# Kernel tuning notes

Hardware: AMD Instinct MI355X
Metric: run time of the kernel (lower is better)

Reference implementation:

```python
import jax, jax.numpy as jnp
import numpy as np

IN_F = 1024
OUT_F = 4096
SEARCH_SPACE = [1, 2, 4, 8, 16]  # block sizes; powers of 2 dividing both dims, capped at 16


def circ_avg(W, bs):
    """Project W [out,in] onto block-circulant structure with block size bs.

    Equivalent to trans_to_cir_meng: within each (bs x bs) block, average each
    wrap-around diagonal and rebuild a circulant block C[k, j] = c[(k - j) % bs].
    """
    q, p = W.shape[0] // bs, W.shape[1] // bs
    t = W.reshape(q, bs, p, bs).transpose(0, 2, 1, 3)  # [q, p, bs, bs]
    i = jnp.arange(bs)
    # rot[..., i, j] = t[..., i, (i + j) % bs]  (rotate rows so diagonals align in columns)
    rot = t[:, :, i[:, None], (i[:, None] + i[None, :]) % bs]  # [q, p, bs, bs]
    c = rot.mean(axis=2)  # [q, p, bs]  mean over each diagonal
    # circulant block: w[..., k, j] = c[..., (k - j) % bs]
    w = c[:, :, (i[:, None] - i[None, :]) % bs]  # [q, p, bs, bs]
    return w.transpose(0, 2, 1, 3).reshape(W.shape)


def setup_inputs() -> dict:
    key = jax.random.key(0)
    k1, k2, k3, k4 = jax.random.split(key, 4)
    x = jax.random.normal(k1, (16, 512, IN_F), dtype=jnp.float32)
    weight = jax.random.normal(k2, (OUT_F, IN_F), dtype=jnp.float32) * 0.02
    alphas = jax.random.normal(k3, (len(SEARCH_SPACE),), dtype=jnp.float32)
    bias = jax.random.normal(k4, (OUT_F,), dtype=jnp.float32) * 0.02
    return {"x": x, "weight": weight, "alphas": alphas, "bias": bias}


def reference(x, weight, alphas, bias):
    # soft NAS mixture over block sizes (tau=1, soft mode)
    a = jax.nn.softmax(alphas)
    W = a[0] * weight  # block_size 1 == original weight
    for idx, bs in enumerate(SEARCH_SPACE[1:], start=1):
        W = W + a[idx] * circ_avg(weight, bs)
    # F.linear: y = x @ W^T + b
    return jnp.einsum("bsi,oi->bso", x, W) + bias
```

## Files before the change

### kernel.cpp

```cpp
#include <hip/hip_runtime.h>

typedef __bf16 bf16;
typedef __bf16 bf16x8 __attribute__((ext_vector_type(8)));
typedef float floatx4 __attribute__((ext_vector_type(4)));

#define IN_F  1024
#define OUT_F 4096
#define M_DIM 8192
#define K_DIM 1024
#define N_DIM 4096

__device__ __forceinline__ unsigned short f2bf(float f) {
    unsigned int u = __float_as_uint(f);
    u += 0x7FFFu + ((u >> 16) & 1u);
    return (unsigned short)(u >> 16);
}

__global__ __launch_bounds__(256) void build_w_kernel(
    const float* __restrict__ W, const float* __restrict__ alphas,
    unsigned short* __restrict__ Wb)
{
    __shared__ __align__(16) float Wl[16 * 256];
    __shared__ __align__(16) float D2[2048];
    __shared__ float D4[1024];
    __shared__ float D8[512];
    __shared__ float D16[256];

    const int t = threadIdx.x;
    const int rb = blockIdx.x >> 2;
    const int cb = blockIdx.x & 3;
    const int row0 = rb * 16, col0 = cb * 256;

    const float4* src = (const float4*)(W + (size_t)row0 * IN_F + col0);
    #pragma unroll
    for (int j = 0; j < 4; ++j) {
        const int idx = j * 256 + t;
        const int r = idx >> 6, c4 = idx & 63;
        ((float4*)Wl)[r * 64 + c4] = src[(size_t)r * 256 + c4];
    }

    float av[5];
    float mx = -1e30f;
    #pragma unroll
    for (int j = 0; j < 5; ++j) { av[j] = alphas[j]; mx = fmaxf(mx, av[j]); }
    float s = 0.f;
    #pragma unroll
    for (int j = 0; j < 5; ++j) { av[j] = __expf(av[j] - mx); s += av[j]; }
    const float inv = 1.f / s;
    #pragma unroll
    for (int j = 0; j < 5; ++j) av[j] *= inv;
    #pragma unroll
    for (int e = 1; e <= 4; ++e) av[e] *= 1.0f / (float)(1 << e);

    __syncthreads();

    {
        const int c16 = t >> 4, d = t & 15;
        float acc = 0.f;
        #pragma unroll
        for (int r = 0; r < 16; ++r)
            acc += Wl[r * 256 + c16 * 16 + ((r + d) & 15)];
        D16[t] = acc;
    }
    #pragma unroll
    for (int it = 0; it < 2; ++it) {
        const int s8 = t + it * 256;
        const int d = s8 & 7, c8 = (s8 >> 3) & 31, r8 = s8 >> 8;
        float acc = 0.f;
        #pragma unroll
        for (int r = 0; r < 8; ++r)
            acc += Wl[(r8 * 8 + r) * 256 + c8 * 8 + ((r + d) & 7)];
        D8[s8] = acc;
    }
    #pragma unroll
    for (int it = 0; it < 4; ++it) {
        const int s4 = t + it * 256;
        const int d = s4 & 3, c4 = (s4 >> 2) & 63, r4 = s4 >> 8;
        float acc = 0.f;
        #pragma unroll
        for (int r = 0; r < 4; ++r)
            acc += Wl[(r4 * 4 + r) * 256 + c4 * 4 + ((r + d) & 3)];
        D4[s4] = acc;
    }
    #pragma unroll
    for (int it = 0; it < 8; ++it) {
        const int s2 = t + it * 256;
        const int d = s2 & 1, c2 = (s2 >> 1) & 127, r2 = s2 >> 8;
        D2[s2] = Wl[(r2 * 2) * 256 + c2 * 2 + d]
               + Wl[(r2 * 2 + 1) * 256 + c2 * 2 + ((1 + d) & 1)];
    }

    __syncthreads();

    const int k = t >> 4, jj = t & 15;
    float res[16];
    #pragma unroll
    for (int jb = 0; jb < 16; ++jb) {
        const int col = jb * 16 + jj;
        const int dd = k - col;
        res[jb] = av[0] * Wl[k * 256 + col]
                + av[1] * D2[((k >> 1) * 128 + (col >> 1)) * 2 + (dd & 1)]
                + av[2] * D4[((k >> 2) * 64  + (col >> 2)) * 4 + (dd & 3)]
                + av[3] * D8[((k >> 3) * 32  + (col >> 3)) * 8 + (dd & 7)]
                + av[4] * D16[(col >> 4) * 16 + (dd & 15)];
    }

    __syncthreads();
    unsigned short* st = (unsigned short*)D2;
    #pragma unroll
    for (int jb = 0; jb < 16; ++jb)
        st[k * 256 + jb * 16 + jj] = f2bf(res[jb]);
    __syncthreads();

    const uint4* p = (const uint4*)(st + k * 256 + jj * 16);
    uint4* dst = (uint4*)(Wb + (size_t)(row0 + k) * IN_F + col0 + jj * 16);
    dst[0] = p[0];
    dst[1] = p[1];
}

__global__ __launch_bounds__(256) void cvt_x_kernel(
    const float* __restrict__ x, uint4* __restrict__ xb)
{
    const int t = blockIdx.x * 256 + threadIdx.x;
    const float4* xv = (const float4*)x;
    const float4 v0 = xv[2 * t];
    const float4 v1 = xv[2 * t + 1];
    uint4 o;
    o.x = (unsigned)f2bf(v0.x) | ((unsigned)f2bf(v0.y) << 16);
    o.y = (unsigned)f2bf(v0.z) | ((unsigned)f2bf(v0.w) << 16);
    o.z = (unsigned)f2bf(v1.x) | ((unsigned)f2bf(v1.y) << 16);
    o.w = (unsigned)f2bf(v1.z) | ((unsigned)f2bf(v1.w) << 16);
    xb[t] = o;
}

__global__ __launch_bounds__(256) void gemm_bt_kernel(
    const bf16* __restrict__ A, const bf16* __restrict__ B,
    const float* __restrict__ bias, float* __restrict__ C)
{
    constexpr int N = N_DIM, K = K_DIM;
    constexpr int TM = 128, TN = 128, TK = 64;
    constexpr int NBLK = (M_DIM / TM) * (N_DIM / TN);

    __shared__ __align__(16) bf16 As[TM * TK];
    __shared__ __align__(16) bf16 Bs[TN * TK];

    const int t    = threadIdx.x;
    const int w    = t >> 6;
    const int l    = t & 63;
    const int quad = l >> 4;
    const int l16  = l & 15;
    const int x7   = l16 & 7;

    const int nb = N / TN;
    const int wgid = (blockIdx.x & 7) * (NBLK >> 3) + (blockIdx.x >> 3);
    const int bm = wgid / nb;
    const int bn = wgid % nb;

    const int wm = (w >> 1) * 64;
    const int wn = (w & 1) * 64;

    floatx4 acc[4][4] = {};

    int crow[4], ccol[4], loff[4];
    #pragma unroll
    for (int q = 0; q < 4; ++q) {
        const int chunk = q * 256 + t;
        crow[q] = chunk >> 3;
        ccol[q] = (((chunk & 7) ^ ((chunk >> 3) & 7)) * 8);
        loff[q] = (q * 256 + (t & ~63)) * 8;
    }

    const bf16* Abase = A + (size_t)bm * TM * K;
    const bf16* Bbase = B + (size_t)bn * TN * K;

    for (int kt = 0; kt < K; kt += TK) {
        #pragma unroll
        for (int q = 0; q < 4; ++q) {
            __builtin_amdgcn_global_load_lds(
                (const __attribute__((address_space(1))) void*)(Abase + (size_t)crow[q] * K + kt + ccol[q]),
                (__attribute__((address_space(3))) void*)(As + loff[q]), 16, 0, 0);
        }
        #pragma unroll
        for (int q = 0; q < 4; ++q) {
            __builtin_amdgcn_global_load_lds(
                (const __attribute__((address_space(1))) void*)(Bbase + (size_t)crow[q] * K + kt + ccol[q]),
                (__attribute__((address_space(3))) void*)(Bs + loff[q]), 16, 0, 0);
        }
        __syncthreads();

        #pragma unroll
        for (int ks = 0; ks < 2; ++ks) {
            bf16x8 af[4], bfr[4];
            const int kx = ((ks * 4 + quad) ^ x7) * 8;
            #pragma unroll
            for (int mt = 0; mt < 4; ++mt)
                af[mt] = *(const bf16x8*)(As + (wm + mt * 16 + l16) * TK + kx);
            #pragma unroll
            for (int nt = 0; nt < 4; ++nt)
                bfr[nt] = *(const bf16x8*)(Bs + (wn + nt * 16 + l16) * TK + kx);
            #pragma unroll
            for (int mt = 0; mt < 4; ++mt)
                #pragma unroll
                for (int nt = 0; nt < 4; ++nt)
                    acc[mt][nt] = __builtin_amdgcn_mfma_f32_16x16x32_bf16(
                        af[mt], bfr[nt], acc[mt][nt], 0, 0, 0);
        }
        __syncthreads();
    }

    float bv[4];
    #pragma unroll
    for (int nt = 0; nt < 4; ++nt)
        bv[nt] = bias[bn * TN + wn + nt * 16 + l16];

    float* Cbase = C + (size_t)(bm * TM + wm) * N + bn * TN + wn;
    #pragma unroll
    for (int mt = 0; mt < 4; ++mt) {
        #pragma unroll
        for (int r = 0; r < 4; ++r) {
            float* crowp = Cbase + (size_t)(mt * 16 + quad * 4 + r) * N;
            #pragma unroll
            for (int nt = 0; nt < 4; ++nt)
                crowp[nt * 16 + l16] = acc[mt][nt][r] + bv[nt];
        }
    }
}

extern "C" void kernel_launch(void* const* d_in, const int* in_sizes, int n_in,
                              void* d_out, int out_size, void* d_ws, size_t ws_size,
                              hipStream_t stream) {
    const float* x      = (const float*)d_in[0];
    const float* weight = (const float*)d_in[1];
    const float* alphas = (const float*)d_in[2];
    const float* bias   = (const float*)d_in[3];
    float* out = (float*)d_out;

    unsigned short* Wb = (unsigned short*)d_ws;
    unsigned short* Xb = (unsigned short*)((char*)d_ws + (size_t)OUT_F * IN_F * 2);

    build_w_kernel<<<(OUT_F / 16) * (IN_F / 256), 256, 0, stream>>>(weight, alphas, Wb);
    cvt_x_kernel<<<(M_DIM * K_DIM / 8) / 256, 256, 0, stream>>>(x, (uint4*)Xb);

    const int grid = (M_DIM / 128) * (N_DIM / 128);
    gemm_bt_kernel<<<grid, 256, 0, stream>>>((const bf16*)Xb, (const bf16*)Wb, bias, out);
}
```

Baseline: 248.4 us.

## Merge prep kernels and rewrite GEMM with 256x128 double-buffered tiles

```diff
diff --git a/kernel.cpp b/kernel.cpp
--- a/kernel.cpp
+++ b/kernel.cpp
@@ -16,17 +16,33 @@
     return (unsigned short)(u >> 16);
 }
 
-__global__ __launch_bounds__(256) void build_w_kernel(
+__global__ __launch_bounds__(256) void prep_kernel(
     const float* __restrict__ W, const float* __restrict__ alphas,
-    unsigned short* __restrict__ Wb)
+    const float* __restrict__ x,
+    unsigned short* __restrict__ Wb, uint4* __restrict__ xb)
 {
+    const int t = threadIdx.x;
+
+    if (blockIdx.x >= 1024) {
+        const int g = (blockIdx.x - 1024) * 256 + t;
+        const float4* xv = (const float4*)x;
+        const float4 v0 = xv[2 * g];
+        const float4 v1 = xv[2 * g + 1];
+        uint4 o;
+        o.x = (unsigned)f2bf(v0.x) | ((unsigned)f2bf(v0.y) << 16);
+        o.y = (unsigned)f2bf(v0.z) | ((unsigned)f2bf(v0.w) << 16);
+        o.z = (unsigned)f2bf(v1.x) | ((unsigned)f2bf(v1.y) << 16);
+        o.w = (unsigned)f2bf(v1.z) | ((unsigned)f2bf(v1.w) << 16);
+        xb[g] = o;
+        return;
+    }
+
     __shared__ __align__(16) float Wl[16 * 256];
     __shared__ __align__(16) float D2[2048];
     __shared__ float D4[1024];
     __shared__ float D8[512];
     __shared__ float D16[256];
 
-    const int t = threadIdx.x;
     const int rb = blockIdx.x >> 2;
     const int cb = blockIdx.x & 3;
     const int row0 = rb * 16, col0 = cb * 256;
@@ -54,8 +70,7 @@
 
     __syncthreads();
 
-    {
-        const int c16 = t >> 4, d = t & 15;
+    {   const int c16 = t >> 4, d = t & 15;
         float acc = 0.f;
         #pragma unroll
         for (int r = 0; r < 16; ++r)
@@ -118,110 +133,130 @@
     dst[1] = p[1];
 }
 
-__global__ __launch_bounds__(256) void cvt_x_kernel(
-    const float* __restrict__ x, uint4* __restrict__ xb)
-{
-    const int t = blockIdx.x * 256 + threadIdx.x;
-    const float4* xv = (const float4*)x;
-    const float4 v0 = xv[2 * t];
-    const float4 v1 = xv[2 * t + 1];
-    uint4 o;
-    o.x = (unsigned)f2bf(v0.x) | ((unsigned)f2bf(v0.y) << 16);
-    o.y = (unsigned)f2bf(v0.z) | ((unsigned)f2bf(v0.w) << 16);
-    o.z = (unsigned)f2bf(v1.x) | ((unsigned)f2bf(v1.y) << 16);
-    o.w = (unsigned)f2bf(v1.z) | ((unsigned)f2bf(v1.w) << 16);
-    xb[t] = o;
-}
-
-__global__ __launch_bounds__(256) void gemm_bt_kernel(
+#define GTM 256
+#define GTN 128
+#define GTK 32
+#define A_EL (GTM * GTK)
+#define B_EL (GTN * GTK)
+#define BUF_EL (A_EL + B_EL)
+
+__global__ __launch_bounds__(256, 3) void gemm_bt_kernel(
     const bf16* __restrict__ A, const bf16* __restrict__ B,
     const float* __restrict__ bias, float* __restrict__ C)
 {
     constexpr int N = N_DIM, K = K_DIM;
-    constexpr int TM = 128, TN = 128, TK = 64;
-    constexpr int NBLK = (M_DIM / TM) * (N_DIM / TN);
-
-    __shared__ __align__(16) bf16 As[TM * TK];
-    __shared__ __align__(16) bf16 Bs[TN * TK];
+    constexpr int NT = K / GTK;
+
+    __shared__ __align__(16) bf16 smem[2 * BUF_EL];
 
     const int t    = threadIdx.x;
     const int w    = t >> 6;
     const int l    = t & 63;
     const int quad = l >> 4;
     const int l16  = l & 15;
-    const int x7   = l16 & 7;
-
-    const int nb = N / TN;
-    const int wgid = (blockIdx.x & 7) * (NBLK >> 3) + (blockIdx.x >> 3);
-    const int bm = wgid / nb;
-    const int bn = wgid % nb;
-
-    const int wm = (w >> 1) * 64;
+
+    const int wm = (w >> 1) * 128;
     const int wn = (w & 1) * 64;
 
-    floatx4 acc[4][4] = {};
-
-    int crow[4], ccol[4], loff[4];
-    #pragma unroll
-    for (int q = 0; q < 4; ++q) {
-        const int chunk = q * 256 + t;
-        crow[q] = chunk >> 3;
-        ccol[q] = (((chunk & 7) ^ ((chunk >> 3) & 7)) * 8);
-        loff[q] = (q * 256 + (t & ~63)) * 8;
-    }
-
-    const bf16* Abase = A + (size_t)bm * TM * K;
-    const bf16* Bbase = B + (size_t)bn * TN * K;
-
-    for (int kt = 0; kt < K; kt += TK) {
+    const int nb = N / GTN;
+    const int bm = blockIdx.x / nb;
+    const int bn = blockIdx.x % nb;
+
+    const int fko = l16 * GTK + ((quad ^ ((l16 >> 1) & 3)) * 8);
+
+    const bf16* Ag[4]; int la[4];
+    const bf16* Bg[2]; int lb[2];
+    {
+        const bf16* Abase = A + (size_t)bm * GTM * K;
+        const bf16* Bbase = B + (size_t)bn * GTN * K;
         #pragma unroll
         for (int q = 0; q < 4; ++q) {
-            __builtin_amdgcn_global_load_lds(
-                (const __attribute__((address_space(1))) void*)(Abase + (size_t)crow[q] * K + kt + ccol[q]),
-                (__attribute__((address_space(3))) void*)(As + loff[q]), 16, 0, 0);
-        }
-        #pragma unroll
-        for (int q = 0; q < 4; ++q) {
-            __builtin_amdgcn_global_load_lds(
-                (const __attribute__((address_space(1))) void*)(Bbase + (size_t)crow[q] * K + kt + ccol[q]),
-                (__attribute__((address_space(3))) void*)(Bs + loff[q]), 16, 0, 0);
-        }
-        __syncthreads();
-
-        #pragma unroll
-        for (int ks = 0; ks < 2; ++ks) {
-            bf16x8 af[4], bfr[4];
-            const int kx = ((ks * 4 + quad) ^ x7) * 8;
+            const int c = q * 256 + t;
+            const int row = c >> 2;
+            const int kq = (c & 3) ^ ((row >> 1) & 3);
+            Ag[q] = Abase + (size_t)row * K + kq * 8;
+            la[q] = (q * 256 + (t & ~63)) * 8;
+        }
+        #pragma unroll
+        for (int q = 0; q < 2; ++q) {
+            const int c = q * 256 + t;
+            const int row = c >> 2;
+            const int kq = (c & 3) ^ ((row >> 1) & 3);
+            Bg[q] = Bbase + (size_t)row * K + kq * 8;
+            lb[q] = (q * 256 + (t & ~63)) * 8;
+        }
+    }
+
+    floatx4 acc[8][4] = {};
+
+#define GLL(SRC, DST)                                                         \
+    __builtin_amdgcn_global_load_lds(                                         \
+        (const __attribute__((address_space(1))) void*)(SRC),                 \
+        (__attribute__((address_space(3))) void*)(DST), 16, 0, 0)
+
+#define STAGE(KOFF, BUFP) do {                                                \
+        _Pragma("unroll")                                                     \
+        for (int q = 0; q < 4; ++q) GLL(Ag[q] + (KOFF), (BUFP) + la[q]);      \
+        _Pragma("unroll")                                                     \
+        for (int q = 0; q < 2; ++q) GLL(Bg[q] + (KOFF), (BUFP) + A_EL + lb[q]); \
+    } while (0)
+
+#define MF(d, va, vb)                                                         \
+    d = __builtin_amdgcn_mfma_f32_16x16x32_bf16(va, vb, d, 0, 0, 0)
+
+    STAGE(0, smem);
+
+    #pragma unroll 1
+    for (int kt = 0; kt < NT; ++kt) {
+        bf16* cur = smem + (kt & 1) * BUF_EL;
+        bf16* nxt = smem + ((kt & 1) ^ 1) * BUF_EL;
+
+        if (kt < NT - 1) {
+            STAGE((kt + 1) * GTK, nxt);
+            asm volatile("s_waitcnt vmcnt(6)" ::: "memory");
+        } else {
+            asm volatile("s_waitcnt vmcnt(0)" ::: "memory");
+        }
+        __builtin_amdgcn_s_barrier();
+
+        bf16x8 af[8], bfr[4];
+        const bf16* a0 = cur + wm * GTK + fko;
+        const bf16* b0 = cur + A_EL + wn * GTK + fko;
+        #pragma unroll
+        for (int n = 0; n < 4; ++n)
+            bfr[n] = *(const bf16x8*)(b0 + n * 16 * GTK);
+        #pragma unroll
+        for (int m = 0; m < 8; ++m)
+            af[m] = *(const bf16x8*)(a0 + m * 16 * GTK);
+
+        __builtin_amdgcn_s_setprio(1);
+        #pragma unroll
+        for (int m = 0; m < 8; ++m)
             #pragma unroll
-            for (int mt = 0; mt < 4; ++mt)
-                af[mt] = *(const bf16x8*)(As + (wm + mt * 16 + l16) * TK + kx);
+            for (int n = 0; n < 4; ++n)
+                MF(acc[m][n], af[m], bfr[n]);
+        __builtin_amdgcn_s_setprio(0);
+
+        __builtin_amdgcn_s_barrier();
+    }
+#undef STAGE
+#undef GLL
+#undef MF
+
+    float bv[4];
+    #pragma unroll
+    for (int nt = 0; nt < 4; ++nt)
+        bv[nt] = bias[bn * GTN + wn + nt * 16 + l16];
+
+    float* Cbase = C + (size_t)(bm * GTM + wm) * N + bn * GTN + wn;
+    #pragma unroll
+    for (int m = 0; m < 8; ++m) {
+        #pragma unroll
+        for (int r = 0; r < 4; ++r) {
+            float* crowp = Cbase + (size_t)(m * 16 + quad * 4 + r) * N;
             #pragma unroll
             for (int nt = 0; nt < 4; ++nt)
-                bfr[nt] = *(const bf16x8*)(Bs + (wn + nt * 16 + l16) * TK + kx);
-            #pragma unroll
-            for (int mt = 0; mt < 4; ++mt)
-                #pragma unroll
-                for (int nt = 0; nt < 4; ++nt)
-                    acc[mt][nt] = __builtin_amdgcn_mfma_f32_16x16x32_bf16(
-                        af[mt], bfr[nt], acc[mt][nt], 0, 0, 0);
-        }
-        __syncthreads();
-    }
-
-    float bv[4];
-    #pragma unroll
-    for (int nt = 0; nt < 4; ++nt)
-        bv[nt] = bias[bn * TN + wn + nt * 16 + l16];
-
-    float* Cbase = C + (size_t)(bm * TM + wm) * N + bn * TN + wn;
-    #pragma unroll
-    for (int mt = 0; mt < 4; ++mt) {
-        #pragma unroll
-        for (int r = 0; r < 4; ++r) {
-            float* crowp = Cbase + (size_t)(mt * 16 + quad * 4 + r) * N;
-            #pragma unroll
-            for (int nt = 0; nt < 4; ++nt)
-                crowp[nt * 16 + l16] = acc[mt][nt][r] + bv[nt];
+                crowp[nt * 16 + l16] = acc[m][nt][r] + bv[nt];
         }
     }
 }
@@ -238,9 +273,8 @@
     unsigned short* Wb = (unsigned short*)d_ws;
     unsigned short* Xb = (unsigned short*)((char*)d_ws + (size_t)OUT_F * IN_F * 2);
 
-    build_w_kernel<<<(OUT_F / 16) * (IN_F / 256), 256, 0, stream>>>(weight, alphas, Wb);
-    cvt_x_kernel<<<(M_DIM * K_DIM / 8) / 256, 256, 0, stream>>>(x, (uint4*)Xb);
-
-    const int grid = (M_DIM / 128) * (N_DIM / 128);
+    prep_kernel<<<1024 + 4096, 256, 0, stream>>>(weight, alphas, x, Wb, (uint4*)Xb);
+
+    const int grid = (M_DIM / GTM) * (N_DIM / GTN);
     gemm_bt_kernel<<<grid, 256, 0, stream>>>((const bf16*)Xb, (const bf16*)Wb, bias, out);
 }
```

Result: slower. 389.0 us (+56.6%).
